# Performance work log

Hardware: AMD Instinct MI355X
Metric: run time of the kernel (lower is better)

## Reference

```python
import jax, jax.numpy as jnp
import numpy as np

B, S, H, FD, FL = 2, 2048, 1024, 3072, 3072
MAX_SPAN = 30
LAM = 0.4
MAX_K = int(S * LAM)  # static upper bound on top-k spans (819)
NEG = -10000.0
LN_EPS = 1e-5


def _mlp(x, W, b, g, be):
    # FullyConnectedLayer: Linear -> GELU(erf) -> LayerNorm (dropout = eval identity)
    h = jax.nn.gelu(x @ W + b, approximate=False)
    mu = jnp.mean(h, axis=-1, keepdims=True)
    var = jnp.var(h, axis=-1, keepdims=True)
    return (h - mu) / jnp.sqrt(var + LN_EPS) * g + be


def _mask_tensor(t, m):
    # s2e mask_tensor: additive -1e4 on masked entries, then clamp
    return jnp.clip(t + (1.0 - m) * NEG, NEG, -NEG)


def setup_inputs() -> dict:
    key = jax.random.key(0)
    ks = iter(jax.random.split(key, 32))
    w = lambda shape: jax.random.normal(next(ks), shape, jnp.float32) * 0.02
    inp = {
        "input_emb": jax.random.normal(next(ks), (B, S, H), jnp.float32),
        "input_masks": jnp.ones((B, S), jnp.int32),
    }
    for p, F in [("sm", FD), ("em", FD), ("sc", FL), ("ec", FL)]:
        inp[p + "_W"] = w((H, F))
        inp[p + "_b"] = jnp.zeros((F,), jnp.float32)
        inp[p + "_g"] = jnp.ones((F,), jnp.float32)
        inp[p + "_be"] = jnp.zeros((F,), jnp.float32)
    inp["cls_s_W"] = w((FD,)); inp["cls_s_b"] = jnp.zeros((), jnp.float32)
    inp["cls_e_W"] = w((FD,)); inp["cls_e_b"] = jnp.zeros((), jnp.float32)
    inp["s2e_W"] = w((FD, FD)); inp["s2e_b"] = jnp.zeros((FD,), jnp.float32)
    for p in ["a_ss", "a_ee", "a_se", "a_es"]:
        inp[p + "_W"] = w((FL, FL))
        inp[p + "_b"] = jnp.zeros((FL,), jnp.float32)
    return inp


def reference(input_emb, input_masks,
              sm_W, sm_b, sm_g, sm_be, em_W, em_b, em_g, em_be,
              sc_W, sc_b, sc_g, sc_be, ec_W, ec_b, ec_g, ec_be,
              cls_s_W, cls_s_b, cls_e_W, cls_e_b, s2e_W, s2e_b,
              a_ss_W, a_ss_b, a_ee_W, a_ee_b, a_se_W, a_se_b, a_es_W, a_es_b):
    # start/end representations
    sm = _mlp(input_emb, sm_W, sm_b, sm_g, sm_be)  # [B,S,FD]
    em = _mlp(input_emb, em_W, em_b, em_g, em_be)  # [B,S,FD]
    sc = _mlp(input_emb, sc_W, sc_b, sc_g, sc_be)  # [B,S,FL]
    ec = _mlp(input_emb, ec_W, ec_b, ec_g, ec_be)  # [B,S,FL]

    # mention scores: joint bilinear + broadcast start/end unary scores
    s_sc = sm @ cls_s_W + cls_s_b  # [B,S]
    e_sc = em @ cls_e_W + cls_e_b  # [B,S]
    joint = jnp.einsum('bsd,btd->bst', sm @ s2e_W + s2e_b, em)  # [B,S,S]
    mention = joint + s_sc[:, :, None] + e_sc[:, None, :]

    # triu(0) & tril(max_span_len-1) band mask
    ii = jnp.arange(S)
    d = ii[None, :] - ii[:, None]  # end - start
    band = ((d >= 0) & (d < MAX_SPAN)).astype(mention.dtype)
    mention = _mask_tensor(mention, band[None])

    # top-k over flattened S*S scores, per-example k via span_mask
    k = (input_masks.sum(-1).astype(jnp.float32) * LAM).astype(jnp.int32)  # [B]
    flat = mention.reshape(B, -1)
    _, top_idx = jax.lax.top_k(flat, MAX_K)  # [B,MAX_K]
    span_mask = (jnp.arange(MAX_K)[None, :] < k[:, None]).astype(jnp.int32)
    idx = top_idx * span_mask + (1 - span_mask) * (S * S - 1)
    sidx = jnp.sort(idx, axis=-1)
    starts = sidx // S  # [B,MAX_K]
    ends = sidx % S
    tms = jnp.take_along_axis(flat, sidx, axis=-1)  # [B,MAX_K]
    pair = tms[:, :, None] + tms[:, None, :]  # [B,MAX_K,MAX_K]

    # gather coref reps at top-k span boundaries
    tks = jnp.take_along_axis(sc, starts[:, :, None], axis=1)  # [B,MAX_K,FL]
    tke = jnp.take_along_axis(ec, ends[:, :, None], axis=1)    # [B,MAX_K,FL]

    coref = (jnp.einsum('bkd,bjd->bkj', tks @ a_ss_W + a_ss_b, tks)
             + jnp.einsum('bkd,bjd->bkj', tke @ a_ee_W + a_ee_b, tke)
             + jnp.einsum('bkd,bjd->bkj', tks @ a_se_W + a_se_b, tke)
             + jnp.einsum('bkd,bjd->bkj', tke @ a_es_W + a_es_b, tks))

    final = pair + coref
    amask = jnp.tril(jnp.ones((MAX_K, MAX_K), final.dtype), -1)[None]
    amask = amask * span_mask[:, :, None].astype(final.dtype)
    final = _mask_tensor(final, amask)
    final = jnp.concatenate([final, jnp.zeros((B, MAX_K, 1), final.dtype)], axis=-1)
    return final
```

## Files before the change

### kernel.cpp

```cpp
#include <hip/hip_runtime.h>
#include <hip/hip_bf16.h>
#include <math.h>

#define S_LEN 2048
#define BATCH 2
#define HDIM 1024
#define FDIM 3072
#define MAXK 819
#define MAXSPAN 30
#define NEGV -10000.0f

typedef __attribute__((ext_vector_type(8))) short short8;
typedef __attribute__((ext_vector_type(4))) float f32x4;
typedef __hip_bfloat16 hb;

__device__ __forceinline__ float gelu_f(float x) {
  return 0.5f * x * (1.0f + erff(x * 0.70710678118654752440f));
}

__device__ __forceinline__ unsigned short bf_bits(float x) {
  hb b = __float2bfloat16(x);
  return *reinterpret_cast<unsigned short*>(&b);
}
__device__ __forceinline__ float bf_back(unsigned short u) {
  hb b = *reinterpret_cast<hb*>(&u);
  return __bfloat162float(b);
}

__device__ __forceinline__ void gload16(const void* g, void* l) {
  __builtin_amdgcn_global_load_lds(
      (const __attribute__((address_space(1))) void*)g,
      (__attribute__((address_space(3))) void*)l, 16, 0, 0);
}

__global__ __launch_bounds__(256) void gemm_fast1(
    const hb* __restrict__ A, const hb* __restrict__ B,
    const float* __restrict__ bias, void* __restrict__ Cv,
    int M, int N, int K, int lda, int ldb, int ldc,
    long long sA, long long sB, long long sC,
    int act, int out_mode, int kspl)
{
  const int zb = blockIdx.z / kspl, zk = blockIdx.z - zb * kspl;
  A += (long long)zb * sA + (long long)zk * K;
  B += (long long)zb * sB + (long long)zk * K;
  const long long cbase = (long long)blockIdx.z * sC;
  const int bm = blockIdx.y * 128, bn = blockIdx.x * 128;
  const int tid = threadIdx.x;
  const int lane = tid & 63;
  const int wv = tid >> 6, wr = wv >> 1, wc = wv & 1;
  const int lrow = lane & 15, lk = lane >> 4;
  __shared__ __align__(16) hb As[128 * 128];
  __shared__ __align__(16) hb Bs[128 * 128];

  const int srow = tid >> 4;
  const int sc8 = tid & 15;
  const int sslot = (sc8 - srow) & 15;

  f32x4 acc[4][4];
#pragma unroll
  for (int mi = 0; mi < 4; ++mi)
#pragma unroll
    for (int ni = 0; ni < 4; ++ni) acc[mi][ni] = (f32x4){0.f, 0.f, 0.f, 0.f};

  long long aoff[8], boff[8];
#pragma unroll
  for (int it = 0; it < 8; ++it) {
    int gm = bm + srow + it * 16; if (gm > M - 1) gm = M - 1;
    int gn = bn + srow + it * 16; if (gn > N - 1) gn = N - 1;
    aoff[it] = (long long)gm * lda + sslot * 8;
    boff[it] = (long long)gn * ldb + sslot * 8;
  }

  for (int k0 = 0; k0 < K; k0 += 128) {
#pragma unroll
    for (int it = 0; it < 8; ++it)
      gload16(A + aoff[it] + k0, &As[(tid + it * 256) * 8]);
#pragma unroll
    for (int it = 0; it < 8; ++it)
      gload16(B + boff[it] + k0, &Bs[(tid + it * 256) * 8]);
    __syncthreads();
#pragma unroll
    for (int ks = 0; ks < 4; ++ks) {
      const int sa = ((ks * 4 + lk + lrow) & 15) * 8;
      short8 a[4], b[4];
#pragma unroll
      for (int mi = 0; mi < 4; ++mi)
        a[mi] = *(const short8*)&As[(wr * 64 + mi * 16 + lrow) * 128 + sa];
#pragma unroll
      for (int ni = 0; ni < 4; ++ni)
        b[ni] = *(const short8*)&Bs[(wc * 64 + ni * 16 + lrow) * 128 + sa];
#pragma unroll
      for (int mi = 0; mi < 4; ++mi)
#pragma unroll
        for (int ni = 0; ni < 4; ++ni)
          acc[mi][ni] = __builtin_amdgcn_mfma_f32_16x16x32_bf16(
              a[mi], b[ni], acc[mi][ni], 0, 0, 0);
    }
    __syncthreads();
  }

  float* Cf = (float*)Cv;
  hb* Cb = (hb*)Cv;
#pragma unroll
  for (int mi = 0; mi < 4; ++mi) {
#pragma unroll
    for (int ni = 0; ni < 4; ++ni) {
#pragma unroll
      for (int q = 0; q < 4; ++q) {
        int gm = bm + wr * 64 + mi * 16 + lk * 4 + q;
        int gn = bn + wc * 64 + ni * 16 + lrow;
        if (gm < M && gn < N) {
          float v = acc[mi][ni][q];
          if (bias) v += bias[gn];
          if (act)  v = gelu_f(v);
          long long off = cbase + (long long)gm * ldc + gn;
          if (out_mode == 1) Cb[off] = __float2bfloat16(v);
          else               Cf[off] = v;
        }
      }
    }
  }
}

__global__ __launch_bounds__(256) void gemm_fast3(
    const hb* __restrict__ Ah, const hb* __restrict__ Al,
    const hb* __restrict__ Bh, const hb* __restrict__ Bl,
    const float* __restrict__ bias, void* __restrict__ Cv, void* __restrict__ Cv2,
    int M, int N, int K, int lda, int ldb, int ldc, int act, int out_mode)
{
  const int bm = blockIdx.y * 128, bn = blockIdx.x * 128;
  const int tid = threadIdx.x;
  const int lane = tid & 63;
  const int wv = tid >> 6, wr = wv >> 1, wc = wv & 1;
  const int lrow = lane & 15, lk = lane >> 4;
  __shared__ __align__(16) hb AsH[128 * 64];
  __shared__ __align__(16) hb AsL[128 * 64];
  __shared__ __align__(16) hb BsH[128 * 64];
  __shared__ __align__(16) hb BsL[128 * 64];

  const int srow = tid >> 3;
  const int sc8 = tid & 7;
  const int sslot = (sc8 - srow) & 7;

  f32x4 acc[4][4];
#pragma unroll
  for (int mi = 0; mi < 4; ++mi)
#pragma unroll
    for (int ni = 0; ni < 4; ++ni) acc[mi][ni] = (f32x4){0.f, 0.f, 0.f, 0.f};

  long long aoff[4], boff[4];
#pragma unroll
  for (int it = 0; it < 4; ++it) {
    int gm = bm + srow + it * 32; if (gm > M - 1) gm = M - 1;
    int gn = bn + srow + it * 32; if (gn > N - 1) gn = N - 1;
    aoff[it] = (long long)gm * lda + sslot * 8;
    boff[it] = (long long)gn * ldb + sslot * 8;
  }

  for (int k0 = 0; k0 < K; k0 += 64) {
#pragma unroll
    for (int it = 0; it < 4; ++it) {
      gload16(Ah + aoff[it] + k0, &AsH[(tid + it * 256) * 8]);
      gload16(Al + aoff[it] + k0, &AsL[(tid + it * 256) * 8]);
      gload16(Bh + boff[it] + k0, &BsH[(tid + it * 256) * 8]);
      gload16(Bl + boff[it] + k0, &BsL[(tid + it * 256) * 8]);
    }
    __syncthreads();
#pragma unroll
    for (int ks = 0; ks < 2; ++ks) {
      const int sa = ((ks * 4 + lk + lrow) & 7) * 8;
      short8 aH[4], aL[4], bH[4], bL[4];
#pragma unroll
      for (int mi = 0; mi < 4; ++mi) {
        int r = (wr * 64 + mi * 16 + lrow) * 64 + sa;
        aH[mi] = *(const short8*)&AsH[r];
        aL[mi] = *(const short8*)&AsL[r];
      }
#pragma unroll
      for (int ni = 0; ni < 4; ++ni) {
        int r = (wc * 64 + ni * 16 + lrow) * 64 + sa;
        bH[ni] = *(const short8*)&BsH[r];
        bL[ni] = *(const short8*)&BsL[r];
      }
#pragma unroll
      for (int mi = 0; mi < 4; ++mi)
#pragma unroll
        for (int ni = 0; ni < 4; ++ni) {
          acc[mi][ni] = __builtin_amdgcn_mfma_f32_16x16x32_bf16(
              aH[mi], bH[ni], acc[mi][ni], 0, 0, 0);
          acc[mi][ni] = __builtin_amdgcn_mfma_f32_16x16x32_bf16(
              aL[mi], bH[ni], acc[mi][ni], 0, 0, 0);
          acc[mi][ni] = __builtin_amdgcn_mfma_f32_16x16x32_bf16(
              aH[mi], bL[ni], acc[mi][ni], 0, 0, 0);
        }
    }
    __syncthreads();
  }

  float* Cf = (float*)Cv;
  hb* Cb = (hb*)Cv;
  hb* Cb2 = (hb*)Cv2;
#pragma unroll
  for (int mi = 0; mi < 4; ++mi) {
#pragma unroll
    for (int ni = 0; ni < 4; ++ni) {
#pragma unroll
      for (int q = 0; q < 4; ++q) {
        int gm = bm + wr * 64 + mi * 16 + lk * 4 + q;
        int gn = bn + wc * 64 + ni * 16 + lrow;
        if (gm < M && gn < N) {
          float v = acc[mi][ni][q];
          if (bias) v += bias[gn];
          if (act)  v = gelu_f(v);
          long long off = (long long)gm * ldc + gn;
          if (out_mode == 2) {
            unsigned short h = bf_bits(v);
            unsigned short l = bf_bits(v - bf_back(h));
            Cb[off] = *reinterpret_cast<hb*>(&h);
            Cb2[off] = *reinterpret_cast<hb*>(&l);
          } else {
            Cf[off] = v;
          }
        }
      }
    }
  }
}

__global__ __launch_bounds__(256) void bandmm(
    const hb* __restrict__ Phi, const hb* __restrict__ Plo,
    const hb* __restrict__ Ehi, const hb* __restrict__ Elo,
    float* __restrict__ partial)
{
  const int s0 = blockIdx.x * 64;
  const int kq = blockIdx.y;
  const int b = blockIdx.z;
  const int tid = threadIdx.x;
  const int lane = tid & 63;
  const int wv = tid >> 6, wr = wv >> 1, wc = wv & 1;
  const int lrow = lane & 15, lk = lane >> 4;
  __shared__ __align__(16) hb As[64 * 64];
  __shared__ __align__(16) hb Bs[96 * 64];

  f32x4 acc[2][3];
#pragma unroll
  for (int mi = 0; mi < 2; ++mi)
#pragma unroll
    for (int ni = 0; ni < 3; ++ni) acc[mi][ni] = (f32x4){0.f, 0.f, 0.f, 0.f};

  const long long Pbase = (long long)(b * S_LEN) * FDIM;
  long long aoff[2], boff[3];
#pragma unroll
  for (int it = 0; it < 2; ++it) {
    int row = (tid + it * 256) >> 3;
    aoff[it] = Pbase + (long long)(s0 + row) * FDIM + (tid & 7) * 8;
  }
#pragma unroll
  for (int it = 0; it < 3; ++it) {
    int row = (tid + it * 256) >> 3;
    int t = s0 + row; if (t > S_LEN - 1) t = S_LEN - 1;
    boff[it] = Pbase + (long long)t * FDIM + (tid & 7) * 8;
  }

  const int kbeg = kq * (FDIM / 4), kend = kbeg + FDIM / 4;
  for (int t3 = 0; t3 < 3; ++t3) {
    const hb* Ap = (t3 == 1) ? Plo : Phi;
    const hb* Bp = (t3 == 2) ? Elo : Ehi;
    for (int k0 = kbeg; k0 < kend; k0 += 64) {
#pragma unroll
      for (int it = 0; it < 2; ++it)
        gload16(Ap + aoff[it] + k0, &As[(tid + it * 256) * 8]);
#pragma unroll
      for (int it = 0; it < 3; ++it)
        gload16(Bp + boff[it] + k0, &Bs[(tid + it * 256) * 8]);
      __syncthreads();
#pragma unroll
      for (int ks = 0; ks < 2; ++ks) {
        short8 a[2], bb[3];
#pragma unroll
        for (int mi = 0; mi < 2; ++mi)
          a[mi] = *(const short8*)&As[(wr * 32 + mi * 16 + lrow) * 64 + ks * 32 + lk * 8];
#pragma unroll
        for (int ni = 0; ni < 3; ++ni)
          bb[ni] = *(const short8*)&Bs[(wc * 48 + ni * 16 + lrow) * 64 + ks * 32 + lk * 8];
#pragma unroll
        for (int mi = 0; mi < 2; ++mi)
#pragma unroll
          for (int ni = 0; ni < 3; ++ni)
            acc[mi][ni] = __builtin_amdgcn_mfma_f32_16x16x32_bf16(
                a[mi], bb[ni], acc[mi][ni], 0, 0, 0);
      }
      __syncthreads();
    }
  }

#pragma unroll
  for (int mi = 0; mi < 2; ++mi) {
#pragma unroll
    for (int ni = 0; ni < 3; ++ni) {
#pragma unroll
      for (int q = 0; q < 4; ++q) {
        int i = wr * 32 + mi * 16 + lk * 4 + q;
        int n = wc * 48 + ni * 16 + lrow;
        int d = n - i;
        if (d >= 0 && d < 32) {
          long long off = (((long long)(kq * 2 + b)) * S_LEN + (s0 + i)) * 32 + d;
          partial[off] = acc[mi][ni][q];
        }
      }
    }
  }
}

__global__ __launch_bounds__(256) void band_reduce(
    const float* __restrict__ partial, const float* __restrict__ ssc,
    const float* __restrict__ esc, float* __restrict__ band)
{
  int idx = blockIdx.x * 256 + threadIdx.x;
  if (idx >= BATCH * S_LEN * 32) return;
  int d = idx & 31;
  int s = (idx >> 5) & (S_LEN - 1);
  int b = idx >> 16;
  int t = s + d;
  float v;
  if (d < MAXSPAN && t < S_LEN) {
    float sum = 0.f;
#pragma unroll
    for (int kq = 0; kq < 4; ++kq)
      sum += partial[(((long long)(kq * 2 + b)) * S_LEN + s) * 32 + d];
    sum += ssc[b * S_LEN + s] + esc[b * S_LEN + t];
    v = fminf(fmaxf(sum, NEGV), -NEGV);
  } else {
    v = -3.0e38f;
  }
  band[idx] = v;
}

__global__ __launch_bounds__(256) void split_mat(
    const float* __restrict__ src, hb* __restrict__ hi, hb* __restrict__ lo,
    long long n4)
{
  long long i = (long long)blockIdx.x * 256 + threadIdx.x;
  if (i >= n4) return;
  float4 v = ((const float4*)src)[i];
  unsigned short h[4], l[4];
  float vv[4] = {v.x, v.y, v.z, v.w};
#pragma unroll
  for (int j = 0; j < 4; ++j) {
    h[j] = bf_bits(vv[j]);
    l[j] = bf_bits(vv[j] - bf_back(h[j]));
  }
  ((uint2*)hi)[i] = *(uint2*)h;
  ((uint2*)lo)[i] = *(uint2*)l;
}

__global__ __launch_bounds__(256) void splitT_mat(
    const float* __restrict__ src, hb* __restrict__ hiT, hb* __restrict__ loT,
    int K, int N)
{
  __shared__ float t[32][33];
  int k0 = blockIdx.y * 32, n0 = blockIdx.x * 32;
  int tx = threadIdx.x & 31, ty = threadIdx.x >> 5;
#pragma unroll
  for (int r = 0; r < 4; ++r)
    t[ty + r * 8][tx] = src[(long long)(k0 + ty + r * 8) * N + (n0 + tx)];
  __syncthreads();
#pragma unroll
  for (int r = 0; r < 4; ++r) {
    int n = n0 + ty + r * 8;
    float v = t[tx][ty + r * 8];
    unsigned short h = bf_bits(v);
    unsigned short l = bf_bits(v - bf_back(h));
    hiT[(long long)n * K + k0 + tx] = *reinterpret_cast<hb*>(&h);
    loT[(long long)n * K + k0 + tx] = *reinterpret_cast<hb*>(&l);
  }
}

__global__ __launch_bounds__(256) void ln_split_dot(
    const float* __restrict__ src, hb* __restrict__ hi, hb* __restrict__ lo,
    const float* __restrict__ g, const float* __restrict__ be,
    const float* __restrict__ w, const float* __restrict__ wb,
    float* __restrict__ dot_out)
{
  __shared__ float row[FDIM];
  __shared__ double scr[4];
  __shared__ double sh_mu, sh_rstd;
  const long long r = blockIdx.x;
  const float* p = src + r * FDIM;
  const int tid = threadIdx.x;

  double s = 0.0;
#pragma unroll
  for (int pp = 0; pp < 3; ++pp) {
    int c4 = pp * 256 + tid;
    float4 v = *(const float4*)(p + c4 * 4);
    *(float4*)&row[c4 * 4] = v;
    s += (double)v.x + (double)v.y + (double)v.z + (double)v.w;
  }
#pragma unroll
  for (int off = 32; off; off >>= 1) s += __shfl_down(s, off, 64);
  if ((tid & 63) == 0) scr[tid >> 6] = s;
  __syncthreads();
  if (tid == 0) sh_mu = (scr[0] + scr[1] + scr[2] + scr[3]) / FDIM;
  __syncthreads();
  double mu = sh_mu;
  double vs = 0.0;
#pragma unroll
  for (int pp = 0; pp < 12; ++pp) {
    double d = (double)row[pp * 256 + tid] - mu;
    vs += d * d;
  }
#pragma unroll
  for (int off = 32; off; off >>= 1) vs += __shfl_down(vs, off, 64);
  __syncthreads();
  if ((tid & 63) == 0) scr[tid >> 6] = vs;
  __syncthreads();
  if (tid == 0)
    sh_rstd = 1.0 / sqrt((scr[0] + scr[1] + scr[2] + scr[3]) / FDIM + 1e-5);
  __syncthreads();
  double rstd = sh_rstd;

  double dot = 0.0;
#pragma unroll
  for (int pp = 0; pp < 3; ++pp) {
    int c4 = pp * 256 + tid;
    float4 gv = *(const float4*)(g + c4 * 4);
    float4 bv = *(const float4*)(be + c4 * 4);
    float4 wv = *(const float4*)(w + c4 * 4);
    float xv[4];
    *(float4*)xv = *(const float4*)&row[c4 * 4];
    unsigned short hh[4], ll[4];
    float gg[4] = {gv.x, gv.y, gv.z, gv.w};
    float bb[4] = {bv.x, bv.y, bv.z, bv.w};
    float ww[4] = {wv.x, wv.y, wv.z, wv.w};
#pragma unroll
    for (int j = 0; j < 4; ++j) {
      float val = (float)(((double)xv[j] - mu) * rstd * (double)gg[j] + (double)bb[j]);
      dot += (double)val * (double)ww[j];
      hh[j] = bf_bits(val);
      ll[j] = bf_bits(val - bf_back(hh[j]));
    }
    *(uint2*)(hi + r * FDIM + c4 * 4) = *(uint2*)hh;
    *(uint2*)(lo + r * FDIM + c4 * 4) = *(uint2*)ll;
  }
#pragma unroll
  for (int off = 32; off; off >>= 1) dot += __shfl_down(dot, off, 64);
  __syncthreads();
  if ((tid & 63) == 0) scr[tid >> 6] = dot;
  __syncthreads();
  if (tid == 0)
    dot_out[r] = (float)(scr[0] + scr[1] + scr[2] + scr[3] + (double)wb[0]);
}

__global__ __launch_bounds__(256) void ln_rows_bf(
    const float* __restrict__ src, hb* __restrict__ dst,
    const float* __restrict__ g, const float* __restrict__ be,
    int n, long long lds_, long long ldd)
{
  long long r = blockIdx.x;
  const float* p = src + r * lds_;
  hb* d = dst + r * ldd;
  __shared__ double scratch[4];
  __shared__ double sh_mu, sh_rstd;
  double s = 0.0;
  for (int c = threadIdx.x; c < n; c += 256) s += (double)p[c];
#pragma unroll
  for (int off = 32; off; off >>= 1) s += __shfl_down(s, off, 64);
  if ((threadIdx.x & 63) == 0) scratch[threadIdx.x >> 6] = s;
  __syncthreads();
  if (threadIdx.x == 0) sh_mu = (scratch[0] + scratch[1] + scratch[2] + scratch[3]) / n;
  __syncthreads();
  double mu = sh_mu;
  double vs = 0.0;
  for (int c = threadIdx.x; c < n; c += 256) { double dd = (double)p[c] - mu; vs += dd * dd; }
#pragma unroll
  for (int off = 32; off; off >>= 1) vs += __shfl_down(vs, off, 64);
  __syncthreads();
  if ((threadIdx.x & 63) == 0) scratch[threadIdx.x >> 6] = vs;
  __syncthreads();
  if (threadIdx.x == 0)
    sh_rstd = 1.0 / sqrt((scratch[0] + scratch[1] + scratch[2] + scratch[3]) / n + 1e-5);
  __syncthreads();
  double rstd = sh_rstd;
  for (int c = threadIdx.x; c < n; c += 256)
    d[c] = __float2bfloat16(
        (float)(((double)p[c] - mu) * rstd * (double)g[c] + (double)be[c]));
}

__device__ __forceinline__ unsigned f2k(float f) {
  unsigned u = __float_as_uint(f);
  return (u & 0x80000000u) ? ~u : (u | 0x80000000u);
}

__device__ void bitonic1024(int* a) {
  const int tid = threadIdx.x;
  for (int sz = 2; sz <= 1024; sz <<= 1) {
    for (int st = sz >> 1; st > 0; st >>= 1) {
      __syncthreads();
      int j = tid ^ st;
      if (j > tid) {
        int x = a[tid], y = a[j];
        bool asc = (tid & sz) == 0;
        if ((x > y) == asc) { a[tid] = y; a[j] = x; }
      }
    }
  }
  __syncthreads();
}

__global__ __launch_bounds__(1024) void select_sort(
    const float* __restrict__ band, const int* __restrict__ masks,
    int* __restrict__ sidx, int* __restrict__ starts, int* __restrict__ ends,
    float* __restrict__ tms, int* __restrict__ kvals)
{
  const int b = blockIdx.x;
  const int tid = threadIdx.x;
  __shared__ int hist[256];
  __shared__ int sel[1024];
  __shared__ int eq[1024];
  __shared__ int sred[16];
  __shared__ int cvar[4];
  __shared__ int cnt_gt, cnt_eq;

  int msum = 0;
  for (int i = tid; i < S_LEN; i += 1024) msum += masks[b * S_LEN + i];
#pragma unroll
  for (int off = 32; off; off >>= 1) msum += __shfl_down(msum, off, 64);
  if ((tid & 63) == 0) sred[tid >> 6] = msum;
  __syncthreads();
  if (tid == 0) {
    int t = 0;
    for (int w = 0; w < 16; ++w) t += sred[w];
    cvar[2] = t;
  }
  __syncthreads();
  int kv = (int)((float)cvar[2] * 0.4f);
  if (kv > MAXK) kv = MAXK;
  if (kv < 0) kv = 0;

  const int NC = S_LEN * MAXSPAN;
  unsigned prefix = 0u;
  int remaining = kv;

  if (kv > 0) {
    for (int byte = 3; byte >= 0; --byte) {
      if (tid < 256) hist[tid] = 0;
      __syncthreads();
      for (int i = tid; i < NC; i += 1024) {
        int s = i / MAXSPAN;
        int d = i - s * MAXSPAN;
        float v = band[((long long)(b * S_LEN + s)) * 32 + d];
        unsigned key = f2k(v);
        bool match = (byte == 3) ||
            ((key >> ((byte + 1) * 8)) == (prefix >> ((byte + 1) * 8)));
        if (match) atomicAdd(&hist[(key >> (byte * 8)) & 255], 1);
      }
      __syncthreads();
      if (tid == 0) {
        int cum = 0, chosen = 255;
        for (int v = 255; v >= 0; --v) {
          int h = hist[v];
          if (cum + h >= remaining) { chosen = v; cvar[0] = remaining - cum; break; }
          cum += h;
        }
        cvar[1] = chosen;
      }
      __syncthreads();
      remaining = cvar[0];
      prefix |= ((unsigned)cvar[1]) << (byte * 8);
      __syncthreads();
    }
    if (tid == 0) { cnt_gt = 0; cnt_eq = 0; }
    __syncthreads();
    for (int i = tid; i < NC; i += 1024) {
      int s = i / MAXSPAN;
      int d = i - s * MAXSPAN;
      float v = band[((long long)(b * S_LEN + s)) * 32 + d];
      unsigned key = f2k(v);
      int flat = s * S_LEN + s + d;
      if (key > prefix) {
        int p = atomicAdd(&cnt_gt, 1);
        if (p < MAXK) sel[p] = flat;
      } else if (key == prefix) {
        int p = atomicAdd(&cnt_eq, 1);
        if (p < 1024) eq[p] = flat;
      }
    }
    __syncthreads();
    int ngt = cnt_gt;
    int neq = cnt_eq; if (neq > 1024) neq = 1024;
    if (tid >= neq) eq[tid] = 0x7FFFFFFF;
    __syncthreads();
    bitonic1024(eq);
    int need = kv - ngt;
    if (tid < need) sel[ngt + tid] = eq[tid];
    __syncthreads();
  }
  if (tid >= kv && tid < MAXK) sel[tid] = S_LEN * S_LEN - 1;
  if (tid >= MAXK) sel[tid] = 0x7FFFFFFF;
  __syncthreads();
  bitonic1024(sel);
  if (tid < MAXK) {
    int idx = sel[tid];
    int s = idx >> 11;
    int t = idx & (S_LEN - 1);
    sidx[b * MAXK + tid] = idx;
    starts[b * MAXK + tid] = s;
    ends[b * MAXK + tid] = t;
    tms[b * MAXK + tid] = band[((long long)(b * S_LEN + s)) * 32 + (t - s)];
  }
  if (tid == 0) kvals[b] = kv;
}

__global__ __launch_bounds__(256) void gather_bf(
    const float* __restrict__ src, const int* __restrict__ rows,
    hb* __restrict__ dst)
{
  int g = blockIdx.x;
  int b = g / MAXK;
  int r = rows[g];
  const float4* s4 = (const float4*)(src + ((long long)(b * S_LEN + r)) * HDIM);
  hb* d = dst + (long long)g * HDIM;
  float4 v = s4[threadIdx.x];
  d[threadIdx.x * 4 + 0] = __float2bfloat16(v.x);
  d[threadIdx.x * 4 + 1] = __float2bfloat16(v.y);
  d[threadIdx.x * 4 + 2] = __float2bfloat16(v.z);
  d[threadIdx.x * 4 + 3] = __float2bfloat16(v.w);
}

__global__ __launch_bounds__(256) void conv_t(
    const float* __restrict__ src, hb* __restrict__ dst,
    int K, int N, int koff, int ldd)
{
  __shared__ float t[32][33];
  int k0 = blockIdx.y * 32, n0 = blockIdx.x * 32;
  int tx = threadIdx.x & 31, ty = threadIdx.x >> 5;
#pragma unroll
  for (int r = 0; r < 4; ++r)
    t[ty + r * 8][tx] = src[(long long)(k0 + ty + r * 8) * N + (n0 + tx)];
  __syncthreads();
#pragma unroll
  for (int r = 0; r < 4; ++r) {
    int n = n0 + ty + r * 8;
    dst[(long long)n * ldd + koff + k0 + tx] = __float2bfloat16(t[tx][ty + r * 8]);
  }
}

__global__ __launch_bounds__(256) void add2(
    const float* __restrict__ a, const float* __restrict__ b,
    float* __restrict__ c, int n)
{
  int i = blockIdx.x * 256 + threadIdx.x;
  if (i < n) c[i] = a[i] + b[i];
}

__global__ __launch_bounds__(256) void final_assemble(
    const float* __restrict__ coref4, const float* __restrict__ tms,
    const int* __restrict__ kvals, float* __restrict__ out)
{
  const long long SL = (long long)MAXK * MAXK;
  int g = blockIdx.x;
  int b = g / MAXK;
  int i = g - b * MAXK;
  int kv = kvals[b];
  float ti = tms[g];
  const float* crow = coref4 + (long long)(b * 4) * SL + (long long)i * MAXK;
  float* orow = out + (long long)b * MAXK * (MAXK + 1) + (long long)i * (MAXK + 1);
  for (int j = threadIdx.x; j < MAXK + 1; j += 256) {
    float v;
    if (j == MAXK) v = 0.f;
    else {
      float c = ((crow[j] + crow[j + SL]) + (crow[j + 2 * SL] + crow[j + 3 * SL]));
      v = ti + tms[b * MAXK + j] + c;
      if (!((j < i) && (i < kv))) v += NEGV;
      v = fminf(fmaxf(v, NEGV), -NEGV);
    }
    orow[j] = v;
  }
}

static inline void launch1(const hb* A, const hb* B, const float* bias, void* C,
    int M, int N, int K, int lda, int ldb, int ldc,
    long long sA, long long sB, long long sC,
    int act, int out_mode, int zcount, int kspl, hipStream_t stream)
{
  dim3 grid((N + 127) / 128, (M + 127) / 128, zcount);
  gemm_fast1<<<grid, 256, 0, stream>>>(A, B, bias, C, M, N, K, lda, ldb, ldc,
                                       sA, sB, sC, act, out_mode, kspl);
}

static inline void launch3(const hb* Ah, const hb* Al, const hb* Bh, const hb* Bl,
    const float* bias, void* C, void* C2, int M, int N, int K,
    int lda, int ldb, int ldc, int act, int out_mode, hipStream_t stream)
{
  dim3 grid((N + 127) / 128, (M + 127) / 128, 1);
  gemm_fast3<<<grid, 256, 0, stream>>>(Ah, Al, Bh, Bl, bias, C, C2,
                                       M, N, K, lda, ldb, ldc, act, out_mode);
}

extern "C" void kernel_launch(void* const* d_in, const int* in_sizes, int n_in,
                              void* d_out, int out_size, void* d_ws, size_t ws_size,
                              hipStream_t stream) {
  const float* input_emb = (const float*)d_in[0];
  const int*   input_masks = (const int*)d_in[1];
  const float* sm_W = (const float*)d_in[2];
  const float* sm_b = (const float*)d_in[3];
  const float* sm_g = (const float*)d_in[4];
  const float* sm_be = (const float*)d_in[5];
  const float* em_W = (const float*)d_in[6];
  const float* em_b = (const float*)d_in[7];
  const float* em_g = (const float*)d_in[8];
  const float* em_be = (const float*)d_in[9];
  const float* sc_W = (const float*)d_in[10];
  const float* sc_b = (const float*)d_in[11];
  const float* sc_g = (const float*)d_in[12];
  const float* sc_be = (const float*)d_in[13];
  const float* ec_W = (const float*)d_in[14];
  const float* ec_b = (const float*)d_in[15];
  const float* ec_g = (const float*)d_in[16];
  const float* ec_be = (const float*)d_in[17];
  const float* cls_s_W = (const float*)d_in[18];
  const float* cls_s_b = (const float*)d_in[19];
  const float* cls_e_W = (const float*)d_in[20];
  const float* cls_e_b = (const float*)d_in[21];
  const float* s2e_W = (const float*)d_in[22];
  const float* s2e_b = (const float*)d_in[23];
  const float* a_ss_W = (const float*)d_in[24];
  const float* a_ss_b = (const float*)d_in[25];
  const float* a_ee_W = (const float*)d_in[26];
  const float* a_ee_b = (const float*)d_in[27];
  const float* a_se_W = (const float*)d_in[28];
  const float* a_se_b = (const float*)d_in[29];
  const float* a_es_W = (const float*)d_in[30];
  const float* a_es_b = (const float*)d_in[31];
  float* out = (float*)d_out;

  const int NROW = BATCH * S_LEN;
  const int MROW = BATCH * MAXK;
  const long long SZ_BIG = (long long)NROW * FDIM * 4;

  char* ws = (char*)d_ws;
  float* smF    = (float*)(ws);
  hb* sm_hi     = (hb*)(ws + 50331648LL);
  hb* sm_lo     = (hb*)(ws + 75497472LL);
  hb* emb_hi    = (hb*)(ws + 100663296LL);
  hb* emb_lo    = (hb*)(ws + 109051904LL);
  hb* w1_hiT    = (hb*)(ws + 117440512LL);
  hb* w1_loT    = (hb*)(ws + 123731968LL);
  hb* s2e_hiT   = (hb*)(ws);
  hb* s2e_loT   = (hb*)(ws + 18874368LL);
  hb* proj_hi   = (hb*)(ws + 100663296LL);
  hb* proj_lo   = (hb*)(ws + 125829120LL);
  hb* emb2_hi   = (hb*)(ws);
  hb* emb2_lo   = (hb*)(ws + 8388608LL);
  hb* w2_hiT    = (hb*)(ws + 16777216LL);
  hb* w2_loT    = (hb*)(ws + 23068672LL);
  float* emF    = (float*)(ws + 50331648LL);
  hb* em_hi     = (hb*)(ws);
  hb* em_lo     = (hb*)(ws + 25165824LL);
  float* partial = (float*)(ws + 50331648LL);
  hb* tkcat = (hb*)(ws);
  hb* qcat  = (hb*)(ws + 20127744LL);
  float* mlp_s = (float*)(ws + 40255488LL);
  float* mlp_e = (float*)(ws + 60383232LL);
  hb* Xs_bf = (hb*)(ws + 80510976LL);
  hb* Xe_bf = (hb*)(ws + 83865600LL);
  hb* scWt  = (hb*)(ws + 87220224LL);
  hb* ecWt  = (hb*)(ws + 93511680LL);
  float* coref4 = (float*)(ws + 99803136LL);
  hb* Wq1t = (hb*)(ws + 40255488LL);
  hb* Wq2t = (hb*)(ws + 78004224LL);
  const long long P = 3 * SZ_BIG;
  float* band = (float*)(ws + P);
  float* ssc  = (float*)(ws + P + 524288);
  float* esc  = (float*)(ws + P + 540672);
  int* sidx   = (int*)(ws + P + 557056);
  int* starts = (int*)(ws + P + 565248);
  int* ends   = (int*)(ws + P + 573440);
  float* tms  = (float*)(ws + P + 581632);
  int* kvals  = (int*)(ws + P + 589824);
  float* biasq1 = (float*)(ws + P + 590080);
  float* biasq2 = (float*)(ws + P + 602368);
  if (ws_size < (size_t)(P + 614656)) return;

  const long long n4_emb = (long long)NROW * HDIM / 4;

  split_mat<<<(int)((n4_emb + 255) / 256), 256, 0, stream>>>(input_emb, emb_hi, emb_lo, n4_emb);
  splitT_mat<<<dim3(FDIM / 32, HDIM / 32), 256, 0, stream>>>(sm_W, w1_hiT, w1_loT, HDIM, FDIM);
  launch3(emb_hi, emb_lo, w1_hiT, w1_loT, sm_b, smF, nullptr,
          NROW, FDIM, HDIM, HDIM, HDIM, FDIM, 1, 0, stream);
  ln_split_dot<<<NROW, 256, 0, stream>>>(smF, sm_hi, sm_lo, sm_g, sm_be,
                                         cls_s_W, cls_s_b, ssc);
  splitT_mat<<<dim3(FDIM / 32, FDIM / 32), 256, 0, stream>>>(s2e_W, s2e_hiT, s2e_loT, FDIM, FDIM);
  launch3(sm_hi, sm_lo, s2e_hiT, s2e_loT, s2e_b, proj_hi, proj_lo,
          NROW, FDIM, FDIM, FDIM, FDIM, FDIM, 0, 2, stream);
  split_mat<<<(int)((n4_emb + 255) / 256), 256, 0, stream>>>(input_emb, emb2_hi, emb2_lo, n4_emb);
  splitT_mat<<<dim3(FDIM / 32, HDIM / 32), 256, 0, stream>>>(em_W, w2_hiT, w2_loT, HDIM, FDIM);
  launch3(emb2_hi, emb2_lo, w2_hiT, w2_loT, em_b, emF, nullptr,
          NROW, FDIM, HDIM, HDIM, HDIM, FDIM, 1, 0, stream);
  ln_split_dot<<<NROW, 256, 0, stream>>>(emF, em_hi, em_lo, em_g, em_be,
                                         cls_e_W, cls_e_b, esc);
  bandmm<<<dim3(S_LEN / 64, 4, BATCH), 256, 0, stream>>>(proj_hi, proj_lo, em_hi, em_lo, partial);
  band_reduce<<<(BATCH * S_LEN * 32) / 256, 256, 0, stream>>>(partial, ssc, esc, band);
  select_sort<<<BATCH, 1024, 0, stream>>>(band, input_masks, sidx, starts, ends, tms, kvals);

  gather_bf<<<MROW, 256, 0, stream>>>(input_emb, starts, Xs_bf);
  gather_bf<<<MROW, 256, 0, stream>>>(input_emb, ends, Xe_bf);

  conv_t<<<dim3(FDIM / 32, HDIM / 32), 256, 0, stream>>>(sc_W, scWt, HDIM, FDIM, 0, HDIM);
  conv_t<<<dim3(FDIM / 32, HDIM / 32), 256, 0, stream>>>(ec_W, ecWt, HDIM, FDIM, 0, HDIM);

  launch1(Xs_bf, scWt, sc_b, mlp_s, MROW, FDIM, HDIM, HDIM, HDIM, FDIM,
          0, 0, 0, 1, 0, 1, 1, stream);
  launch1(Xe_bf, ecWt, ec_b, mlp_e, MROW, FDIM, HDIM, HDIM, HDIM, FDIM,
          0, 0, 0, 1, 0, 1, 1, stream);

  ln_rows_bf<<<MROW, 256, 0, stream>>>(mlp_s, tkcat, sc_g, sc_be, FDIM, FDIM, 2 * FDIM);
  ln_rows_bf<<<MROW, 256, 0, stream>>>(mlp_e, tkcat + FDIM, ec_g, ec_be, FDIM, FDIM, 2 * FDIM);

  conv_t<<<dim3(FDIM / 32, FDIM / 32), 256, 0, stream>>>(a_ss_W, Wq1t, FDIM, FDIM, 0,    2 * FDIM);
  conv_t<<<dim3(FDIM / 32, FDIM / 32), 256, 0, stream>>>(a_es_W, Wq1t, FDIM, FDIM, FDIM, 2 * FDIM);
  conv_t<<<dim3(FDIM / 32, FDIM / 32), 256, 0, stream>>>(a_se_W, Wq2t, FDIM, FDIM, 0,    2 * FDIM);
  conv_t<<<dim3(FDIM / 32, FDIM / 32), 256, 0, stream>>>(a_ee_W, Wq2t, FDIM, FDIM, FDIM, 2 * FDIM);
  add2<<<FDIM / 256, 256, 0, stream>>>(a_ss_b, a_es_b, biasq1, FDIM);
  add2<<<FDIM / 256, 256, 0, stream>>>(a_se_b, a_ee_b, biasq2, FDIM);

  launch1(tkcat, Wq1t, biasq1, qcat, MROW, 2 * FDIM, 2 * FDIM,
          2 * FDIM, 2 * FDIM, 2 * FDIM, 0, 0, 0, 0, 1, 1, 1, stream);

  launch1(qcat, tkcat, nullptr, coref4, MAXK, MAXK, 1536,
          2 * FDIM, 2 * FDIM, MAXK,
          (long long)MAXK * 2 * FDIM, (long long)MAXK * 2 * FDIM,
          (long long)MAXK * MAXK, 0, 0, BATCH * 4, 4, stream);

  final_assemble<<<MROW, 256, 0, stream>>>(coref4, tms, kvals, out);
}
```

Measured before the change: 1.268 ms.

## Replace split-bf16 GEMM with 256x256 double-buffered pipelined 8-wave kernel

Replaces the 128x128 four-array split-precision GEMM with a 256x256-tile, 512-thread kernel. The hi/lo products run as three sequential K segments (AhBh, AlBh, AhBl) over a single double-buffered LDS tile. Global loads for upcoming tiles are interleaved with MFMA phases, using explicit barriers, waitcnt and setprio, so memory traffic overlaps compute. Bounds checks are removed, so M and N are assumed to be multiples of 256, and the larger tile reduces the number of blocks in the grid.

```diff
diff --git a/kernel.cpp b/kernel.cpp
--- a/kernel.cpp
+++ b/kernel.cpp
@@ -122,105 +122,205 @@
   }
 }
 
-__global__ __launch_bounds__(256) void gemm_fast3(
+struct TS { const hb* a; const hb* b; int kk; };
+__device__ __forceinline__ TS tsrc(int tt, int ntK,
+    const hb* Ah, const hb* Al, const hb* Bh, const hb* Bl)
+{
+  int seg = (tt >= ntK) + (tt >= 2 * ntK);
+  TS r;
+  r.kk = (tt - seg * ntK) << 6;
+  r.a = (seg == 1) ? Al : Ah;
+  r.b = (seg == 2) ? Bl : Bh;
+  return r;
+}
+
+#define STG(srcp, base, ldx, ldsp, h, kk) do {                               \
+    const hb* _g = (srcp) + (base) + (long long)((h) * 128) * (ldx) + (kk);  \
+    gload16(_g, (ldsp) + (h) * 8192 + tid * 8);                              \
+    gload16(_g + 64LL * (ldx), (ldsp) + (h) * 8192 + 4096 + tid * 8);        \
+  } while (0)
+
+__global__ __launch_bounds__(512) void gemm8(
     const hb* __restrict__ Ah, const hb* __restrict__ Al,
     const hb* __restrict__ Bh, const hb* __restrict__ Bl,
-    const float* __restrict__ bias, void* __restrict__ Cv, void* __restrict__ Cv2,
-    int M, int N, int K, int lda, int ldb, int ldc, int act, int out_mode)
-{
-  const int bm = blockIdx.y * 128, bn = blockIdx.x * 128;
+    const float* __restrict__ bias, void* __restrict__ Cv,
+    void* __restrict__ Cv2,
+    int M, int N, int K, int lda, int ldb, int ldc,
+    int act, int out_mode, int nseg)
+{
+  const int bm = blockIdx.y * 256, bn = blockIdx.x * 256;
   const int tid = threadIdx.x;
   const int lane = tid & 63;
-  const int wv = tid >> 6, wr = wv >> 1, wc = wv & 1;
+  const int wv = tid >> 6, wr = wv >> 2, wc = wv & 3;
   const int lrow = lane & 15, lk = lane >> 4;
-  __shared__ __align__(16) hb AsH[128 * 64];
-  __shared__ __align__(16) hb AsL[128 * 64];
-  __shared__ __align__(16) hb BsH[128 * 64];
-  __shared__ __align__(16) hb BsL[128 * 64];
+  const int ntK = K >> 6;
+  const int NT = nseg * ntK;
+
+  __shared__ __align__(16) hb As[2][256 * 64];
+  __shared__ __align__(16) hb Bs[2][256 * 64];
 
   const int srow = tid >> 3;
-  const int sc8 = tid & 7;
-  const int sslot = (sc8 - srow) & 7;
-
-  f32x4 acc[4][4];
-#pragma unroll
-  for (int mi = 0; mi < 4; ++mi)
+  const int sslot = ((tid & 7) - srow) & 7;
+  const long long baseA = (long long)(bm + srow) * lda + sslot * 8;
+  const long long baseB = (long long)(bn + srow) * ldb + sslot * 8;
+
+  const int raBase = wr * 128 + lrow;
+  const int rbBase = wc * 64 + lrow;
+  const int psk0 = ((lk + lrow) & 7) * 8;
+  const int psk1 = ((4 + lk + lrow) & 7) * 8;
+
+  f32x4 acc[8][4];
+#pragma unroll
+  for (int mi = 0; mi < 8; ++mi)
 #pragma unroll
     for (int ni = 0; ni < 4; ++ni) acc[mi][ni] = (f32x4){0.f, 0.f, 0.f, 0.f};
 
-  long long aoff[4], boff[4];
-#pragma unroll
-  for (int it = 0; it < 4; ++it) {
-    int gm = bm + srow + it * 32; if (gm > M - 1) gm = M - 1;
-    int gn = bn + srow + it * 32; if (gn > N - 1) gn = N - 1;
-    aoff[it] = (long long)gm * lda + sslot * 8;
-    boff[it] = (long long)gn * ldb + sslot * 8;
-  }
-
-  for (int k0 = 0; k0 < K; k0 += 64) {
-#pragma unroll
-    for (int it = 0; it < 4; ++it) {
-      gload16(Ah + aoff[it] + k0, &AsH[(tid + it * 256) * 8]);
-      gload16(Al + aoff[it] + k0, &AsL[(tid + it * 256) * 8]);
-      gload16(Bh + boff[it] + k0, &BsH[(tid + it * 256) * 8]);
-      gload16(Bl + boff[it] + k0, &BsL[(tid + it * 256) * 8]);
-    }
-    __syncthreads();
-#pragma unroll
-    for (int ks = 0; ks < 2; ++ks) {
-      const int sa = ((ks * 4 + lk + lrow) & 7) * 8;
-      short8 aH[4], aL[4], bH[4], bL[4];
-#pragma unroll
-      for (int mi = 0; mi < 4; ++mi) {
-        int r = (wr * 64 + mi * 16 + lrow) * 64 + sa;
-        aH[mi] = *(const short8*)&AsH[r];
-        aL[mi] = *(const short8*)&AsL[r];
-      }
-#pragma unroll
-      for (int ni = 0; ni < 4; ++ni) {
-        int r = (wc * 64 + ni * 16 + lrow) * 64 + sa;
-        bH[ni] = *(const short8*)&BsH[r];
-        bL[ni] = *(const short8*)&BsL[r];
-      }
-#pragma unroll
-      for (int mi = 0; mi < 4; ++mi)
-#pragma unroll
-        for (int ni = 0; ni < 4; ++ni) {
-          acc[mi][ni] = __builtin_amdgcn_mfma_f32_16x16x32_bf16(
-              aH[mi], bH[ni], acc[mi][ni], 0, 0, 0);
-          acc[mi][ni] = __builtin_amdgcn_mfma_f32_16x16x32_bf16(
-              aL[mi], bH[ni], acc[mi][ni], 0, 0, 0);
-          acc[mi][ni] = __builtin_amdgcn_mfma_f32_16x16x32_bf16(
-              aH[mi], bL[ni], acc[mi][ni], 0, 0, 0);
-        }
-    }
-    __syncthreads();
+  {
+    TS t0 = tsrc(0, ntK, Ah, Al, Bh, Bl);
+    STG(t0.a, baseA, lda, &As[0][0], 0, t0.kk);
+    STG(t0.a, baseA, lda, &As[0][0], 1, t0.kk);
+    STG(t0.b, baseB, ldb, &Bs[0][0], 0, t0.kk);
+    STG(t0.b, baseB, ldb, &Bs[0][0], 1, t0.kk);
+    if (NT > 1) {
+      TS t1 = tsrc(1, ntK, Ah, Al, Bh, Bl);
+      STG(t1.a, baseA, lda, &As[1][0], 0, t1.kk);
+      STG(t1.a, baseA, lda, &As[1][0], 1, t1.kk);
+      asm volatile("s_waitcnt vmcnt(4)" ::: "memory");
+    } else {
+      asm volatile("s_waitcnt vmcnt(0)" ::: "memory");
+    }
+    __builtin_amdgcn_s_barrier();
+  }
+
+  short8 a0[4][2], a1[4][2], b0[2][2], b1[2][2];
+
+  for (int t = 0; t < NT; ++t) {
+    const int bf = t & 1;
+    const hb* Ab = &As[bf][0];
+    const hb* Bb = &Bs[bf][0];
+    hb* AbW = &As[bf][0];
+    hb* BbN = &Bs[bf ^ 1][0];
+    const TS n1 = tsrc(t + 1, ntK, Ah, Al, Bh, Bl);
+    const TS n2 = tsrc(t + 2, ntK, Ah, Al, Bh, Bl);
+    const bool st1 = (t + 1 < NT), st2 = (t + 2 < NT);
+
+#pragma unroll
+    for (int mi = 0; mi < 4; ++mi) {
+      const int ra = (raBase + mi * 16) * 64;
+      a0[mi][0] = *(const short8*)&Ab[ra + psk0];
+      a0[mi][1] = *(const short8*)&Ab[ra + psk1];
+    }
+#pragma unroll
+    for (int ni = 0; ni < 2; ++ni) {
+      const int rb = (rbBase + ni * 16) * 64;
+      b0[ni][0] = *(const short8*)&Bb[rb + psk0];
+      b0[ni][1] = *(const short8*)&Bb[rb + psk1];
+    }
+    if (st1) STG(n1.b, baseB, ldb, BbN, 0, n1.kk);
+    __builtin_amdgcn_s_barrier();
+    asm volatile("s_waitcnt lgkmcnt(0)" ::: "memory");
+    __builtin_amdgcn_sched_barrier(0);
+    __builtin_amdgcn_s_setprio(1);
+#pragma unroll
+    for (int mi = 0; mi < 4; ++mi)
+#pragma unroll
+      for (int ni = 0; ni < 2; ++ni) {
+        acc[mi][ni] = __builtin_amdgcn_mfma_f32_16x16x32_bf16(
+            a0[mi][0], b0[ni][0], acc[mi][ni], 0, 0, 0);
+        acc[mi][ni] = __builtin_amdgcn_mfma_f32_16x16x32_bf16(
+            a0[mi][1], b0[ni][1], acc[mi][ni], 0, 0, 0);
+      }
+    __builtin_amdgcn_s_setprio(0);
+    __builtin_amdgcn_s_barrier();
+
+#pragma unroll
+    for (int mi = 0; mi < 4; ++mi) {
+      const int ra = (raBase + (4 + mi) * 16) * 64;
+      a1[mi][0] = *(const short8*)&Ab[ra + psk0];
+      a1[mi][1] = *(const short8*)&Ab[ra + psk1];
+    }
+    if (st1) STG(n1.b, baseB, ldb, BbN, 1, n1.kk);
+    __builtin_amdgcn_s_barrier();
+    asm volatile("s_waitcnt lgkmcnt(0)" ::: "memory");
+    __builtin_amdgcn_sched_barrier(0);
+    __builtin_amdgcn_s_setprio(1);
+#pragma unroll
+    for (int mi = 0; mi < 4; ++mi)
+#pragma unroll
+      for (int ni = 0; ni < 2; ++ni) {
+        acc[4 + mi][ni] = __builtin_amdgcn_mfma_f32_16x16x32_bf16(
+            a1[mi][0], b0[ni][0], acc[4 + mi][ni], 0, 0, 0);
+        acc[4 + mi][ni] = __builtin_amdgcn_mfma_f32_16x16x32_bf16(
+            a1[mi][1], b0[ni][1], acc[4 + mi][ni], 0, 0, 0);
+      }
+    __builtin_amdgcn_s_setprio(0);
+    __builtin_amdgcn_s_barrier();
+
+#pragma unroll
+    for (int ni = 0; ni < 2; ++ni) {
+      const int rb = (rbBase + (2 + ni) * 16) * 64;
+      b1[ni][0] = *(const short8*)&Bb[rb + psk0];
+      b1[ni][1] = *(const short8*)&Bb[rb + psk1];
+    }
+    if (st2) STG(n2.a, baseA, lda, AbW, 0, n2.kk);
+    __builtin_amdgcn_s_barrier();
+    asm volatile("s_waitcnt lgkmcnt(0)" ::: "memory");
+    __builtin_amdgcn_sched_barrier(0);
+    __builtin_amdgcn_s_setprio(1);
+#pragma unroll
+    for (int mi = 0; mi < 4; ++mi)
+#pragma unroll
+      for (int ni = 0; ni < 2; ++ni) {
+        acc[mi][2 + ni] = __builtin_amdgcn_mfma_f32_16x16x32_bf16(
+            a0[mi][0], b1[ni][0], acc[mi][2 + ni], 0, 0, 0);
+        acc[mi][2 + ni] = __builtin_amdgcn_mfma_f32_16x16x32_bf16(
+            a0[mi][1], b1[ni][1], acc[mi][2 + ni], 0, 0, 0);
+      }
+    __builtin_amdgcn_s_setprio(0);
+    __builtin_amdgcn_s_barrier();
+
+    if (st2) STG(n2.a, baseA, lda, AbW, 1, n2.kk);
+    __builtin_amdgcn_s_barrier();
+    __builtin_amdgcn_s_setprio(1);
+#pragma unroll
+    for (int mi = 0; mi < 4; ++mi)
+#pragma unroll
+      for (int ni = 0; ni < 2; ++ni) {
+        acc[4 + mi][2 + ni] = __builtin_amdgcn_mfma_f32_16x16x32_bf16(
+            a1[mi][0], b1[ni][0], acc[4 + mi][2 + ni], 0, 0, 0);
+        acc[4 + mi][2 + ni] = __builtin_amdgcn_mfma_f32_16x16x32_bf16(
+            a1[mi][1], b1[ni][1], acc[4 + mi][2 + ni], 0, 0, 0);
+      }
+    __builtin_amdgcn_s_setprio(0);
+    if (st2) asm volatile("s_waitcnt vmcnt(4)" ::: "memory");
+    else     asm volatile("s_waitcnt vmcnt(0)" ::: "memory");
+    __builtin_amdgcn_s_barrier();
   }
 
   float* Cf = (float*)Cv;
   hb* Cb = (hb*)Cv;
   hb* Cb2 = (hb*)Cv2;
 #pragma unroll
-  for (int mi = 0; mi < 4; ++mi) {
+  for (int mi = 0; mi < 8; ++mi) {
 #pragma unroll
     for (int ni = 0; ni < 4; ++ni) {
 #pragma unroll
       for (int q = 0; q < 4; ++q) {
-        int gm = bm + wr * 64 + mi * 16 + lk * 4 + q;
-        int gn = bn + wc * 64 + ni * 16 + lrow;
-        if (gm < M && gn < N) {
-          float v = acc[mi][ni][q];
-          if (bias) v += bias[gn];
-          if (act)  v = gelu_f(v);
-          long long off = (long long)gm * ldc + gn;
-          if (out_mode == 2) {
-            unsigned short h = bf_bits(v);
-            unsigned short l = bf_bits(v - bf_back(h));
-            Cb[off] = *reinterpret_cast<hb*>(&h);
-            Cb2[off] = *reinterpret_cast<hb*>(&l);
-          } else {
-            Cf[off] = v;
-          }
+        const int gm = bm + wr * 128 + mi * 16 + lk * 4 + q;
+        const int gn = bn + wc * 64 + ni * 16 + lrow;
+        float v = acc[mi][ni][q];
+        if (bias) v += bias[gn];
+        if (act)  v = gelu_f(v);
+        const long long off = (long long)gm * ldc + gn;
+        if (out_mode == 2) {
+          unsigned short h = bf_bits(v);
+          unsigned short l = bf_bits(v - bf_back(h));
+          Cb[off] = *reinterpret_cast<hb*>(&h);
+          Cb2[off] = *reinterpret_cast<hb*>(&l);
+        } else if (out_mode == 1) {
+          Cb[off] = __float2bfloat16(v);
+        } else {
+          Cf[off] = v;
         }
       }
     }
@@ -689,13 +789,13 @@
                                        sA, sB, sC, act, out_mode, kspl);
 }
 
-static inline void launch3(const hb* Ah, const hb* Al, const hb* Bh, const hb* Bl,
+static inline void launch8(const hb* Ah, const hb* Al, const hb* Bh, const hb* Bl,
     const float* bias, void* C, void* C2, int M, int N, int K,
-    int lda, int ldb, int ldc, int act, int out_mode, hipStream_t stream)
-{
-  dim3 grid((N + 127) / 128, (M + 127) / 128, 1);
-  gemm_fast3<<<grid, 256, 0, stream>>>(Ah, Al, Bh, Bl, bias, C, C2,
-                                       M, N, K, lda, ldb, ldc, act, out_mode);
+    int lda, int ldb, int ldc, int act, int out_mode, int nseg, hipStream_t stream)
+{
+  dim3 grid(N / 256, M / 256, 1);
+  gemm8<<<grid, 512, 0, stream>>>(Ah, Al, Bh, Bl, bias, C, C2,
+                                  M, N, K, lda, ldb, ldc, act, out_mode, nseg);
 }
 
 extern "C" void kernel_launch(void* const* d_in, const int* in_sizes, int n_in,
@@ -787,17 +887,17 @@
 
   split_mat<<<(int)((n4_emb + 255) / 256), 256, 0, stream>>>(input_emb, emb_hi, emb_lo, n4_emb);
   splitT_mat<<<dim3(FDIM / 32, HDIM / 32), 256, 0, stream>>>(sm_W, w1_hiT, w1_loT, HDIM, FDIM);
-  launch3(emb_hi, emb_lo, w1_hiT, w1_loT, sm_b, smF, nullptr,
-          NROW, FDIM, HDIM, HDIM, HDIM, FDIM, 1, 0, stream);
+  launch8(emb_hi, emb_lo, w1_hiT, w1_loT, sm_b, smF, nullptr,
+          NROW, FDIM, HDIM, HDIM, HDIM, FDIM, 1, 0, 3, stream);
   ln_split_dot<<<NROW, 256, 0, stream>>>(smF, sm_hi, sm_lo, sm_g, sm_be,
                                          cls_s_W, cls_s_b, ssc);
   splitT_mat<<<dim3(FDIM / 32, FDIM / 32), 256, 0, stream>>>(s2e_W, s2e_hiT, s2e_loT, FDIM, FDIM);
-  launch3(sm_hi, sm_lo, s2e_hiT, s2e_loT, s2e_b, proj_hi, proj_lo,
-          NROW, FDIM, FDIM, FDIM, FDIM, FDIM, 0, 2, stream);
+  launch8(sm_hi, sm_lo, s2e_hiT, s2e_loT, s2e_b, proj_hi, proj_lo,
+          NROW, FDIM, FDIM, FDIM, FDIM, FDIM, 0, 2, 3, stream);
   split_mat<<<(int)((n4_emb + 255) / 256), 256, 0, stream>>>(input_emb, emb2_hi, emb2_lo, n4_emb);
   splitT_mat<<<dim3(FDIM / 32, HDIM / 32), 256, 0, stream>>>(em_W, w2_hiT, w2_loT, HDIM, FDIM);
-  launch3(emb2_hi, emb2_lo, w2_hiT, w2_loT, em_b, emF, nullptr,
-          NROW, FDIM, HDIM, HDIM, HDIM, FDIM, 1, 0, stream);
+  launch8(emb2_hi, emb2_lo, w2_hiT, w2_loT, em_b, emF, nullptr,
+          NROW, FDIM, HDIM, HDIM, HDIM, FDIM, 1, 0, 3, stream);
   ln_split_dot<<<NROW, 256, 0, stream>>>(emF, em_hi, em_lo, em_g, em_be,
                                          cls_e_W, cls_e_b, esc);
   bandmm<<<dim3(S_LEN / 64, 4, BATCH), 256, 0, stream>>>(proj_hi, proj_lo, em_hi, em_lo, partial);
```

After: 1.407 ms. 1.11x slower.
